# Kernel optimization log

Measured on AMD Instinct MI355X. Metric: run time of the kernel, lower is better.

The kernel has to match this reference:

```python
import jax, jax.numpy as jnp
import numpy as np

T, B, N, C, H, D = 4, 8, 1024, 512, 8, 64
EPS = 1e-5


def setup_inputs() -> dict:
    key = jax.random.key(0)
    ks = jax.random.split(key, 16)
    d = {"x": jax.random.normal(ks[0], (T, B, N, C), jnp.float32)}
    for i, nm in enumerate(["q", "k", "v", "p"]):
        kW, kmu, kvar = jax.random.split(ks[1 + i], 3)
        d[f"W{nm}"] = jax.random.normal(kW, (C, C), jnp.float32) * 0.02
        d[f"b{nm}"] = jnp.zeros((C,), jnp.float32)
        d[f"g{nm}"] = jnp.ones((C,), jnp.float32)
        d[f"beta{nm}"] = jnp.zeros((C,), jnp.float32)
        d[f"mu{nm}"] = jax.random.normal(kmu, (C,), jnp.float32) * 0.1
        d[f"var{nm}"] = jax.random.uniform(kvar, (C,), jnp.float32, 0.5, 1.5)
    return d


def _lin_bn(z, W, b, g, beta, mu, var):
    # nn.Linear over channel dim, then eval-mode BatchNorm1d per channel
    y = jnp.einsum('tbnc,dc->tbnd', z, W) + b
    return (y - mu) * (g * jax.lax.rsqrt(var + EPS)) + beta


def _to_heads(z):
    # (t,b,n,c) -> (t,b,h,n,d)
    return z.reshape(T, B, N, H, D).transpose(0, 1, 3, 2, 4)


def reference(x, Wq, bq, gq, betaq, muq, varq,
              Wk, bk, gk, betak, muk, vark,
              Wv, bv, gv, betav, muv, varv,
              Wp, bp, gp, betap, mup, varp):
    q = _to_heads(_lin_bn(x, Wq, bq, gq, betaq, muq, varq))
    k = _to_heads(_lin_bn(x, Wk, bk, gk, betak, muk, vark))
    v = _to_heads(_lin_bn(x, Wv, bv, gv, betav, muv, varv))
    # attention_linear variant: kv = (k^T @ v) / N ; y = q @ kv
    kv = jnp.einsum('tbhnd,tbhne->tbhde', k, v) / float(N)  # (t,b,h,d,d)
    y = jnp.einsum('tbhnd,tbhde->tbhne', q, kv)             # (t,b,h,n,d)
    y = y.transpose(0, 1, 3, 2, 4).reshape(T, B, N, C)
    return _lin_bn(y, Wp, bp, gp, betap, mup, varp)
```

## Files before the change

kernel.cpp:

```cpp
#include <hip/hip_runtime.h>

#define T_ 4
#define B_ 8
#define N_ 1024
#define C_ 512
#define H_ 8
#define D_ 64
#define M_ (T_*B_*N_)
#define TB_ (T_*B_)

typedef __bf16 bf16;
typedef __bf16 bf16x4 __attribute__((ext_vector_type(4)));
typedef __bf16 bf16x8 __attribute__((ext_vector_type(8)));
typedef float f32x4 __attribute__((ext_vector_type(4)));

__device__ __forceinline__ void gload16(const void* g, void* l) {
  __builtin_amdgcn_global_load_lds(
      (const __attribute__((address_space(1))) void*)g,
      (__attribute__((address_space(3))) void*)l, 16, 0, 0);
}

struct PtrPack { const float* p[24]; };

__global__ __launch_bounds__(256)
void cvt_prep(PtrPack pk, const float* __restrict__ x, bf16* __restrict__ xb,
              bf16* __restrict__ xT, float* __restrict__ spart,
              bf16* __restrict__ WB, float* __restrict__ BS,
              bf16* __restrict__ WqT) {
  const int t = threadIdx.x;
  __shared__ __align__(16) char smem[21120];
  if (blockIdx.x < 4096) {
    const int bid = blockIdx.x;
    const int tb = bid >> 7, nc = (bid >> 3) & 15, cc = bid & 7;
    float* lds = (float*)smem;
    float* sred = (float*)smem + 4160;
    const float* xbase = x + (size_t)tb * 524288 + (size_t)nc * 64 * 512 + cc * 64;
    bf16* xbb = xb + (size_t)tb * 524288 + (size_t)nc * 64 * 512 + cc * 64;
    bf16* xTb = xT + (size_t)tb * 524288 + (size_t)(cc * 64) * 1024 + nc * 64;
    const int rgrp = t >> 4, k = t & 15;
    float s0 = 0, s1 = 0, s2 = 0, s3 = 0;
#pragma unroll
    for (int p = 0; p < 4; p++) {
      int r = p * 16 + rgrp;
      float4 v = *(const float4*)(xbase + (size_t)r * 512 + k * 4);
      bf16x4 o; o[0]=(bf16)v.x; o[1]=(bf16)v.y; o[2]=(bf16)v.z; o[3]=(bf16)v.w;
      *(bf16x4*)(xbb + (size_t)r * 512 + k * 4) = o;
      lds[r*65 + k*4+0]=v.x; lds[r*65 + k*4+1]=v.y;
      lds[r*65 + k*4+2]=v.z; lds[r*65 + k*4+3]=v.w;
      s0 += v.x; s1 += v.y; s2 += v.z; s3 += v.w;
    }
    sred[rgrp*64 + k*4+0]=s0; sred[rgrp*64 + k*4+1]=s1;
    sred[rgrp*64 + k*4+2]=s2; sred[rgrp*64 + k*4+3]=s3;
    __syncthreads();
#pragma unroll
    for (int p = 0; p < 16; p++) {
      int c = p * 4 + (t >> 6), n = t & 63;
      xTb[(size_t)c * 1024 + n] = (bf16)lds[n*65 + c];
    }
    if (t < 64) {
      float tot = 0;
#pragma unroll
      for (int rg = 0; rg < 16; rg++) tot += sred[rg*64 + t];
      spart[(size_t)((tb*8 + cc)*16 + nc) * 64 + t] = tot;
    }
    return;
  }
  if (blockIdx.x < 6144) {
    const int e = blockIdx.x - 4096;
    const int mat = e >> 9, d = e & 511;
    const float* W    = pk.p[6*mat + 0];
    const float* b    = pk.p[6*mat + 1];
    const float* g    = pk.p[6*mat + 2];
    const float* beta = pk.p[6*mat + 3];
    const float* mu   = pk.p[6*mat + 4];
    const float* var  = pk.p[6*mat + 5];
    float s = g[d] * rsqrtf(var[d] + 1e-5f);
    if (t == 0) BS[mat*512 + d] = (b[d] - mu[d]) * s + beta[d];
    bf16* Wout = WB + (size_t)mat * 262144 + (size_t)d * 512;
    for (int c = t; c < 512; c += 256)
      Wout[c] = (bf16)(W[(size_t)d * 512 + c] * s);
    return;
  }
  const int e = blockIdx.x - 6144;
  const int di = e >> 3, ci = e & 7;
  float* lds = (float*)smem;
  const float* W = pk.p[0];
  const float* g = pk.p[2];
  const float* var = pk.p[5];
  const int rgrp = t >> 4, k = t & 15;
#pragma unroll
  for (int p = 0; p < 4; p++) {
    int r = p * 16 + rgrp;
    int d = di * 64 + r;
    float s = g[d] * rsqrtf(var[d] + 1e-5f);
    float4 v = *(const float4*)(W + (size_t)d * 512 + ci * 64 + k * 4);
    lds[r*65 + k*4+0] = v.x * s; lds[r*65 + k*4+1] = v.y * s;
    lds[r*65 + k*4+2] = v.z * s; lds[r*65 + k*4+3] = v.w * s;
  }
  __syncthreads();
#pragma unroll
  for (int p = 0; p < 16; p++) {
    int c = p * 4 + (t >> 6), dd = t & 63;
    WqT[(size_t)(ci*64 + c) * 512 + di*64 + dd] = (bf16)lds[dd*65 + c];
  }
}

__global__ __launch_bounds__(256)
void gram_ksvs(const bf16* __restrict__ xT, const bf16* __restrict__ WB,
               const float* __restrict__ spart, bf16* __restrict__ Gb,
               float* __restrict__ ksv) {
  const int t = threadIdx.x;
  __shared__ __align__(16) char smem[24576];
  if (blockIdx.x >= 640) {
    const int e = blockIdx.x - 640, tb = e >> 1, m = e & 1;
    float* sl = (float*)smem;
#pragma unroll
    for (int half = 0; half < 2; half++) {
      int c = t + half * 256, cc = c >> 6, cl = c & 63;
      float tot = 0;
#pragma unroll
      for (int ncf = 0; ncf < 16; ncf++)
        tot += spart[(size_t)((tb*8 + cc)*16 + ncf) * 64 + cl];
      sl[c] = tot;
    }
    __syncthreads();
#pragma unroll
    for (int half = 0; half < 2; half++) {
      int d = t + half * 256;
      const bf16* Wrow = WB + (size_t)(m + 1) * 262144 + (size_t)d * 512;
      float acc = 0;
      for (int k = 0; k < 512; k += 8) {
        bf16x8 wv = *(const bf16x8*)(Wrow + k);
#pragma unroll
        for (int i = 0; i < 8; i++) acc += (float)wv[i] * sl[k + i];
      }
      ksv[m * 16384 + tb * 512 + d] = acc;
    }
    return;
  }
  constexpr int K = 1024;
  const int bid = blockIdx.x;
  const int xcd = bid & 7, j9 = bid >> 3;
  const int bat = xcd + 8 * (j9 / 20);
  const int tile = j9 % 20;
  int mi, ni;
  if (tile < 8)       { mi = tile;          ni = 0; }
  else if (tile < 14) { mi = tile - 8 + 2;  ni = 1; }
  else if (tile < 18) { mi = tile - 14 + 4; ni = 2; }
  else                { mi = tile - 18 + 6; ni = 3; }
  const bf16* A = xT + (size_t)bat * 524288;
  const int m0 = mi * 64, n0 = ni * 128;
  bf16* As = (bf16*)smem;
  bf16* Bs = (bf16*)(smem + 8192);
  const int w = t >> 6, l = t & 63;
  const int wm = w >> 1, wn = w & 1;
  const int lr = l & 15, lq = l >> 4, l7 = l & 7, lh = l >> 3;
  const int srcc = (l7 ^ lh) * 8;
  f32x4 acc[2][4] = {};
  for (int kt = 0; kt < 16; kt++) {
#pragma unroll
    for (int i = 0; i < 2; i++) {
      int rb = w * 16 + i * 8;
      gload16(A + (size_t)(m0 + rb + lh) * K + kt * 64 + srcc, &As[rb * 64]);
    }
#pragma unroll
    for (int i = 0; i < 4; i++) {
      int rb = w * 32 + i * 8;
      gload16(A + (size_t)(n0 + rb + lh) * K + kt * 64 + srcc, &Bs[rb * 64]);
    }
    __syncthreads();
    bf16x8 af[2][2], bv[4][2];
#pragma unroll
    for (int f = 0; f < 2; f++) {
      int ra = wm * 32 + f * 16 + lr;
#pragma unroll
      for (int s = 0; s < 2; s++)
        af[f][s] = *(const bf16x8*)&As[ra * 64 + (((s*4+lq) ^ (ra & 7)) * 8)];
    }
#pragma unroll
    for (int f = 0; f < 4; f++) {
      int rb2 = wn * 64 + f * 16 + lr;
#pragma unroll
      for (int s = 0; s < 2; s++)
        bv[f][s] = *(const bf16x8*)&Bs[rb2 * 64 + (((s*4+lq) ^ (rb2 & 7)) * 8)];
    }
#pragma unroll
    for (int mt = 0; mt < 2; mt++)
#pragma unroll
      for (int nt = 0; nt < 4; nt++)
#pragma unroll
        for (int s = 0; s < 2; s++)
          acc[mt][nt] = __builtin_amdgcn_mfma_f32_16x16x32_bf16(
              af[mt][s], bv[nt][s], acc[mt][nt], 0, 0, 0);
    __syncthreads();
  }
  bf16* ob = Gb + (size_t)bat * 262144;
#pragma unroll
  for (int mt = 0; mt < 2; mt++)
#pragma unroll
    for (int nt = 0; nt < 4; nt++) {
      int j = n0 + wn * 64 + nt * 16 + lr;
      size_t mrow = (size_t)m0 + wm * 32 + mt * 16 + lq * 4;
#pragma unroll
      for (int r = 0; r < 4; r++)
        ob[(mrow + r) * 512 + j] = (bf16)acc[mt][nt][r];
    }
  bf16* TB = (bf16*)smem;
#pragma unroll
  for (int mt = 0; mt < 2; mt++)
#pragma unroll
    for (int nt = 0; nt < 4; nt++) {
      int a = wn * 64 + nt * 16 + lr;
#pragma unroll
      for (int r = 0; r < 4; r++) {
        int b = wm * 32 + mt * 16 + lq * 4 + r;
        TB[(a * 64 + b) ^ ((a & 7) << 3)] = (bf16)acc[mt][nt][r];
      }
    }
  __syncthreads();
  const int rowa = t >> 1, half = t & 1;
#pragma unroll
  for (int i = 0; i < 4; i++) {
    int c8 = half * 4 + i;
    bf16x8 v = *(const bf16x8*)&TB[(rowa * 64 + c8 * 8) ^ ((rowa & 7) << 3)];
    *(bf16x8*)(ob + (size_t)(n0 + rowa) * 512 + m0 + c8 * 8) = v;
  }
}

template <int NKT, int MTILES, bool BF16OUT, bool BIAS>
__global__ __launch_bounds__(256, 6)
void gemm_n(const bf16* __restrict__ Abase, size_t Astr,
            const bf16* __restrict__ Btbase, size_t Btstr,
            const float* __restrict__ BSb,
            bf16* __restrict__ ob, float* __restrict__ of, size_t Ostr) {
  constexpr int K = NKT * 64;
  constexpr int PERB = MTILES * 4;
  const int bid = blockIdx.x;
  const int xcd = bid & 7, j9 = bid >> 3;
  const int bat = xcd + 8 * (j9 / PERB);
  const int tile = j9 % PERB;
  const int mi = tile >> 2, ni = tile & 3;
  const bf16* A = Abase + (size_t)bat * Astr;
  const bf16* Bt = Btbase + (size_t)bat * Btstr;
  const int m0 = mi * 64, n0 = ni * 128;
  __shared__ __align__(16) bf16 As[64][64];
  __shared__ __align__(16) bf16 Bs[128][64];
  const int tid = threadIdx.x, w = tid >> 6, l = tid & 63;
  const int wm = w >> 1, wn = w & 1;
  const int lr = l & 15, lq = l >> 4, l7 = l & 7, lh = l >> 3;
  const int srcc = (l7 ^ lh) * 8;
  f32x4 acc[2][4] = {};
  for (int kt = 0; kt < NKT; kt++) {
#pragma unroll
    for (int i = 0; i < 2; i++) {
      int rb = w * 16 + i * 8;
      gload16(A + (size_t)(m0 + rb + lh) * K + kt * 64 + srcc, &As[rb][0]);
    }
#pragma unroll
    for (int i = 0; i < 4; i++) {
      int rb = w * 32 + i * 8;
      gload16(Bt + (size_t)(n0 + rb + lh) * K + kt * 64 + srcc, &Bs[rb][0]);
    }
    __syncthreads();
    bf16x8 af[2][2], bv[4][2];
#pragma unroll
    for (int f = 0; f < 2; f++) {
      int ra = wm * 32 + f * 16 + lr;
#pragma unroll
      for (int s = 0; s < 2; s++)
        af[f][s] = *(const bf16x8*)&As[ra][((s*4+lq) ^ (ra & 7)) * 8];
    }
#pragma unroll
    for (int f = 0; f < 4; f++) {
      int rb2 = wn * 64 + f * 16 + lr;
#pragma unroll
      for (int s = 0; s < 2; s++)
        bv[f][s] = *(const bf16x8*)&Bs[rb2][((s*4+lq) ^ (rb2 & 7)) * 8];
    }
#pragma unroll
    for (int mt = 0; mt < 2; mt++)
#pragma unroll
      for (int nt = 0; nt < 4; nt++)
#pragma unroll
        for (int s = 0; s < 2; s++)
          acc[mt][nt] = __builtin_amdgcn_mfma_f32_16x16x32_bf16(
              af[mt][s], bv[nt][s], acc[mt][nt], 0, 0, 0);
    __syncthreads();
  }

  float bja[4];
  if constexpr (BIAS) {
#pragma unroll
    for (int nt = 0; nt < 4; nt++) {
      int j = n0 + wn * 64 + nt * 16 + lr;
      bja[nt] = BSb[(size_t)bat * 512 + j];
    }
  }
#pragma unroll
  for (int mt = 0; mt < 2; mt++)
#pragma unroll
    for (int nt = 0; nt < 4; nt++) {
      int j = n0 + wn * 64 + nt * 16 + lr;
      size_t mrow = (size_t)m0 + wm * 32 + mt * 16 + lq * 4;
#pragma unroll
      for (int r = 0; r < 4; r++) {
        if constexpr (BF16OUT)
          ob[(size_t)bat * Ostr + (mrow + r) * 512 + j] = (bf16)acc[mt][nt][r];
        else
          of[(size_t)bat * Ostr + (mrow + r) * 512 + j] =
              acc[mt][nt][r] + (BIAS ? bja[nt] : 0.f);
      }
    }
}

__global__ __launch_bounds__(256, 6)
void gemm_vtc(const bf16* __restrict__ ZT, const bf16* __restrict__ WqT,
              const float* __restrict__ BS, const float* __restrict__ cpart,
              bf16* __restrict__ VT, float* __restrict__ cvec) {
  constexpr int K = 512;
  const int tid = threadIdx.x;
  if (blockIdx.x >= 1024) {
    const int tb = blockIdx.x - 1024;
#pragma unroll
    for (int half = 0; half < 2; half++) {
      int j = tid + half * 256;
      float s = BS[1536 + j];
#pragma unroll
      for (int h = 0; h < 8; h++) s += cpart[(size_t)(tb * 8 + h) * 512 + j];
      cvec[tb * 512 + j] = s;
    }
    return;
  }
  const int bid = blockIdx.x;
  const int xcd = bid & 7, j9 = bid >> 3;
  const int bat = xcd + 8 * (j9 >> 5);
  const int tile = j9 & 31;
  const int mi = tile >> 2, ni = tile & 3;
  const bf16* A = ZT + (size_t)bat * 262144;
  const int m0 = mi * 64, n0 = ni * 128;
  __shared__ __align__(16) bf16 As[64][64];
  __shared__ __align__(16) bf16 Bs[128][64];
  const int w = tid >> 6, l = tid & 63;
  const int wm = w >> 1, wn = w & 1;
  const int lr = l & 15, lq = l >> 4, l7 = l & 7, lh = l >> 3;
  const int srcc = (l7 ^ lh) * 8;
  f32x4 acc[2][4] = {};
  for (int kt = 0; kt < 8; kt++) {
#pragma unroll
    for (int i = 0; i < 2; i++) {
      int rb = w * 16 + i * 8;
      gload16(A + (size_t)(m0 + rb + lh) * K + kt * 64 + srcc, &As[rb][0]);
    }
#pragma unroll
    for (int i = 0; i < 4; i++) {
      int rb = w * 32 + i * 8;
      gload16(WqT + (size_t)(n0 + rb + lh) * K + kt * 64 + srcc, &Bs[rb][0]);
    }
    __syncthreads();
    bf16x8 af[2][2], bv[4][2];
#pragma unroll
    for (int f = 0; f < 2; f++) {
      int ra = wm * 32 + f * 16 + lr;
#pragma unroll
      for (int s = 0; s < 2; s++)
        af[f][s] = *(const bf16x8*)&As[ra][((s*4+lq) ^ (ra & 7)) * 8];
    }
#pragma unroll
    for (int f = 0; f < 4; f++) {
      int rb2 = wn * 64 + f * 16 + lr;
#pragma unroll
      for (int s = 0; s < 2; s++)
        bv[f][s] = *(const bf16x8*)&Bs[rb2][((s*4+lq) ^ (rb2 & 7)) * 8];
    }
#pragma unroll
    for (int mt = 0; mt < 2; mt++)
#pragma unroll
      for (int nt = 0; nt < 4; nt++)
#pragma unroll
        for (int s = 0; s < 2; s++)
          acc[mt][nt] = __builtin_amdgcn_mfma_f32_16x16x32_bf16(
              af[mt][s], bv[nt][s], acc[mt][nt], 0, 0, 0);
    __syncthreads();
  }
#pragma unroll
  for (int mt = 0; mt < 2; mt++)
#pragma unroll
    for (int nt = 0; nt < 4; nt++) {
      int j = n0 + wn * 64 + nt * 16 + lr;
      size_t mrow = (size_t)m0 + wm * 32 + mt * 16 + lq * 4;
#pragma unroll
      for (int r = 0; r < 4; r++)
        VT[(size_t)bat * 262144 + (mrow + r) * 512 + j] = (bf16)acc[mt][nt][r];
    }
}

__global__ __launch_bounds__(256)
void kvz(const bf16* __restrict__ KGb, const bf16* __restrict__ WB,
         const float* __restrict__ BS, const float* __restrict__ ksv,
         bf16* __restrict__ ZT, float* __restrict__ cpart) {
  const int gid = blockIdx.x, tb = gid >> 3, h = gid & 7;
  const int t = threadIdx.x, w = t >> 6, l = t & 63;
  const int lr = l & 15, lq = l >> 4;
  __shared__ __align__(16) bf16 kvb[4096];

  const bf16* KGrow = KGb + (size_t)tb * 262144 + (size_t)(64*h) * 512;
  const bf16* Vrow  = WB + 2u * 262144 + (size_t)(64*h) * 512;

  f32x4 acc2[4] = {};
  for (int ks = 0; ks < 16; ks++) {
    const int kc = ks * 32 + lq * 8;
    bf16x8 bv = *(const bf16x8*)(Vrow + (size_t)(w*16 + lr) * 512 + kc);
#pragma unroll
    for (int mf = 0; mf < 4; mf++) {
      bf16x8 af = *(const bf16x8*)(KGrow + (size_t)(mf*16 + lr) * 512 + kc);
      acc2[mf] = __builtin_amdgcn_mfma_f32_16x16x32_bf16(af, bv, acc2[mf], 0, 0, 0);
    }
  }
  {
    const float inv = 1.f / 1024.f;
    const int e = w * 16 + lr;
    const float vsh = ksv[16384 + tb * 512 + 64*h + e];
    const float bvh = BS[1024 + 64*h + e];
#pragma unroll
    for (int mf = 0; mf < 4; mf++)
#pragma unroll
      for (int r = 0; r < 4; r++) {
        int d = mf * 16 + lq * 4 + r;
        float ksh = ksv[tb * 512 + 64*h + d];
        float bkh = BS[512 + 64*h + d];
        float kv = (acc2[mf][r] + ksh * bvh + bkh * vsh) * inv + bkh * bvh;
        kvb[d * 64 + ((((e >> 3) ^ (d & 7)) * 8) + (e & 7))] = (bf16)kv;
      }
  }
  __syncthreads();

  f32x4 acc3[4][8] = {};
#pragma unroll
  for (int s = 0; s < 2; s++) {
    bf16x8 af3[4];
#pragma unroll
    for (int mf = 0; mf < 4; mf++) {
      int d = mf * 16 + lr;
      af3[mf] = *(const bf16x8*)&kvb[d * 64 + (((s*4+lq) ^ (d & 7)) * 8)];
    }
#pragma unroll
    for (int nf = 0; nf < 8; nf++) {
      int jj = w * 128 + nf * 16 + lr;
      bf16x8 b3 = *(const bf16x8*)(WB + 3u * 262144 + (size_t)jj * 512 +
                                   64*h + s * 32 + lq * 8);
#pragma unroll
      for (int mf = 0; mf < 4; mf++)
        acc3[mf][nf] = __builtin_amdgcn_mfma_f32_16x16x32_bf16(
            af3[mf], b3, acc3[mf][nf], 0, 0, 0);
    }
  }

  bf16* zbase = ZT + (size_t)tb * 262144 + 64*h;
#pragma unroll
  for (int nf = 0; nf < 8; nf++) {
    int jj = w * 128 + nf * 16 + lr;
    float cp = 0.f;
#pragma unroll
    for (int mf = 0; mf < 4; mf++) {
      bf16x4 o;
#pragma unroll
      for (int r = 0; r < 4; r++) {
        o[r] = (bf16)acc3[mf][nf][r];
        cp += acc3[mf][nf][r] * BS[64*h + mf*16 + lq*4 + r];
      }
      *(bf16x4*)(zbase + (size_t)jj * 512 + mf * 16 + lq * 4) = o;
    }
    cp += __shfl_xor(cp, 16);
    cp += __shfl_xor(cp, 32);
    if (lq == 0) cpart[(size_t)(tb * 8 + h) * 512 + jj] = cp;
  }
}

extern "C" void kernel_launch(void* const* d_in, const int* in_sizes, int n_in,
                              void* d_out, int out_size, void* d_ws, size_t ws_size,
                              hipStream_t stream) {
  const float* x = (const float*)d_in[0];
  char* ws = (char*)d_ws;
  bf16*  xb    = (bf16*)(ws + 0);
  bf16*  xT    = (bf16*)(ws + 33554432);
  bf16*  Gb    = (bf16*)(ws + 67108864);
  bf16*  KGb   = (bf16*)(ws + 83886080);
  bf16*  ZT    = (bf16*)(ws + 100663296);
  bf16*  VT    = (bf16*)(ws + 117440512);
  bf16*  WB    = (bf16*)(ws + 134217728);
  bf16*  WqT   = (bf16*)(ws + 136314880);
  float* BS    = (float*)(ws + 136839168);
  float* ksv   = (float*)(ws + 136847360);
  float* cpart = (float*)(ws + 136978432);
  float* cvec  = (float*)(ws + 137502720);
  float* spart = (float*)(ws + 137568256);
  (void)in_sizes; (void)n_in; (void)out_size; (void)ws_size;

  PtrPack pk;
  for (int i = 0; i < 24; i++) pk.p[i] = (const float*)d_in[1 + i];

  cvt_prep<<<6208, 256, 0, stream>>>(pk, x, xb, xT, spart, WB, BS, WqT);
  gram_ksvs<<<704, 256, 0, stream>>>(xT, WB, spart, Gb, ksv);
  gemm_n<8, 8, true, false><<<1024, 256, 0, stream>>>(
      WB + 262144, 0, Gb, 262144, nullptr, KGb, nullptr, 262144);
  kvz<<<256, 256, 0, stream>>>(KGb, WB, BS, ksv, ZT, cpart);
  gemm_vtc<<<1056, 256, 0, stream>>>(ZT, WqT, BS, cpart, VT, cvec);
  gemm_n<8, 16, false, true><<<2048, 256, 0, stream>>>(
      xb, 524288, VT, 262144, cvec, nullptr, (float*)d_out, 524288);
}
```

Measured before the change: 135.7 us.

## Fuse fp32-to-bf16 conversion of x into final output GEMM

```diff
diff --git a/kernel.cpp b/kernel.cpp
--- a/kernel.cpp
+++ b/kernel.cpp
@@ -23,7 +23,7 @@
 struct PtrPack { const float* p[24]; };
 
 __global__ __launch_bounds__(256)
-void cvt_prep(PtrPack pk, const float* __restrict__ x, bf16* __restrict__ xb,
+void cvt_prep(PtrPack pk, const float* __restrict__ x,
               bf16* __restrict__ xT, float* __restrict__ spart,
               bf16* __restrict__ WB, float* __restrict__ BS,
               bf16* __restrict__ WqT) {
@@ -35,7 +35,6 @@
     float* lds = (float*)smem;
     float* sred = (float*)smem + 4160;
     const float* xbase = x + (size_t)tb * 524288 + (size_t)nc * 64 * 512 + cc * 64;
-    bf16* xbb = xb + (size_t)tb * 524288 + (size_t)nc * 64 * 512 + cc * 64;
     bf16* xTb = xT + (size_t)tb * 524288 + (size_t)(cc * 64) * 1024 + nc * 64;
     const int rgrp = t >> 4, k = t & 15;
     float s0 = 0, s1 = 0, s2 = 0, s3 = 0;
@@ -43,8 +42,6 @@
     for (int p = 0; p < 4; p++) {
       int r = p * 16 + rgrp;
       float4 v = *(const float4*)(xbase + (size_t)r * 512 + k * 4);
-      bf16x4 o; o[0]=(bf16)v.x; o[1]=(bf16)v.y; o[2]=(bf16)v.z; o[3]=(bf16)v.w;
-      *(bf16x4*)(xbb + (size_t)r * 512 + k * 4) = o;
       lds[r*65 + k*4+0]=v.x; lds[r*65 + k*4+1]=v.y;
       lds[r*65 + k*4+2]=v.z; lds[r*65 + k*4+3]=v.w;
       s0 += v.x; s1 += v.y; s2 += v.z; s3 += v.w;
@@ -313,6 +310,89 @@
     }
 }
 
+__global__ __launch_bounds__(256, 5)
+void gemm_ox(const float* __restrict__ x, const bf16* __restrict__ VTb,
+             const float* __restrict__ cvec, float* __restrict__ of) {
+  constexpr int K = 512, NKT = 8, PERB = 64;
+  const int bid = blockIdx.x;
+  const int xcd = bid & 7, j9 = bid >> 3;
+  const int bat = xcd + 8 * (j9 / PERB);
+  const int tile = j9 % PERB;
+  const int mi = tile >> 2, ni = tile & 3;
+  const float* A = x + (size_t)bat * 524288;
+  const bf16* Bt = VTb + (size_t)bat * 262144;
+  const int m0 = mi * 64, n0 = ni * 128;
+  __shared__ __align__(16) bf16 As[64][64];
+  __shared__ __align__(16) bf16 Bs[128][64];
+  const int tid = threadIdx.x, w = tid >> 6, l = tid & 63;
+  const int wm = w >> 1, wn = w & 1;
+  const int lr = l & 15, lq = l >> 4, l7 = l & 7, lh = l >> 3;
+  const int srcc = (l7 ^ lh) * 8;
+  const int ach = tid & 7;
+  const int arow = tid >> 3;
+  f32x4 acc[2][4] = {};
+  for (int kt = 0; kt < NKT; kt++) {
+#pragma unroll
+    for (int i = 0; i < 2; i++) {
+      int r = i * 32 + arow;
+      const float* src = A + (size_t)(m0 + r) * 512 + kt * 64 + ach * 8;
+      float4 v0 = *(const float4*)(src);
+      float4 v1 = *(const float4*)(src + 4);
+      bf16x8 o;
+      o[0]=(bf16)v0.x; o[1]=(bf16)v0.y; o[2]=(bf16)v0.z; o[3]=(bf16)v0.w;
+      o[4]=(bf16)v1.x; o[5]=(bf16)v1.y; o[6]=(bf16)v1.z; o[7]=(bf16)v1.w;
+      *(bf16x8*)&As[r][((ach ^ (r & 7)) * 8)] = o;
+    }
+#pragma unroll
+    for (int i = 0; i < 4; i++) {
+      int rb = w * 32 + i * 8;
+      gload16(Bt + (size_t)(n0 + rb + lh) * K + kt * 64 + srcc, &Bs[rb][0]);
+    }
+    __syncthreads();
+    bf16x8 af[2][2], bv[4][2];
+#pragma unroll
+    for (int f = 0; f < 2; f++) {
+      int ra = wm * 32 + f * 16 + lr;
+#pragma unroll
+      for (int s = 0; s < 2; s++)
+        af[f][s] = *(const bf16x8*)&As[ra][((s*4+lq) ^ (ra & 7)) * 8];
+    }
+#pragma unroll
+    for (int f = 0; f < 4; f++) {
+      int rb2 = wn * 64 + f * 16 + lr;
+#pragma unroll
+      for (int s = 0; s < 2; s++)
+        bv[f][s] = *(const bf16x8*)&Bs[rb2][((s*4+lq) ^ (rb2 & 7)) * 8];
+    }
+#pragma unroll
+    for (int mt = 0; mt < 2; mt++)
+#pragma unroll
+      for (int nt = 0; nt < 4; nt++)
+#pragma unroll
+        for (int s = 0; s < 2; s++)
+          acc[mt][nt] = __builtin_amdgcn_mfma_f32_16x16x32_bf16(
+              af[mt][s], bv[nt][s], acc[mt][nt], 0, 0, 0);
+    __syncthreads();
+  }
+
+  float bja[4];
+#pragma unroll
+  for (int nt = 0; nt < 4; nt++) {
+    int j = n0 + wn * 64 + nt * 16 + lr;
+    bja[nt] = cvec[(size_t)bat * 512 + j];
+  }
+#pragma unroll
+  for (int mt = 0; mt < 2; mt++)
+#pragma unroll
+    for (int nt = 0; nt < 4; nt++) {
+      int j = n0 + wn * 64 + nt * 16 + lr;
+      size_t mrow = (size_t)m0 + wm * 32 + mt * 16 + lq * 4;
+#pragma unroll
+      for (int r = 0; r < 4; r++)
+        of[(size_t)bat * 524288 + (mrow + r) * 512 + j] = acc[mt][nt][r] + bja[nt];
+    }
+}
+
 __global__ __launch_bounds__(256, 6)
 void gemm_vtc(const bf16* __restrict__ ZT, const bf16* __restrict__ WqT,
               const float* __restrict__ BS, const float* __restrict__ cpart,
@@ -481,7 +561,6 @@
                               hipStream_t stream) {
   const float* x = (const float*)d_in[0];
   char* ws = (char*)d_ws;
-  bf16*  xb    = (bf16*)(ws + 0);
   bf16*  xT    = (bf16*)(ws + 33554432);
   bf16*  Gb    = (bf16*)(ws + 67108864);
   bf16*  KGb   = (bf16*)(ws + 83886080);
@@ -499,12 +578,11 @@
   PtrPack pk;
   for (int i = 0; i < 24; i++) pk.p[i] = (const float*)d_in[1 + i];
 
-  cvt_prep<<<6208, 256, 0, stream>>>(pk, x, xb, xT, spart, WB, BS, WqT);
+  cvt_prep<<<6208, 256, 0, stream>>>(pk, x, xT, spart, WB, BS, WqT);
   gram_ksvs<<<704, 256, 0, stream>>>(xT, WB, spart, Gb, ksv);
   gemm_n<8, 8, true, false><<<1024, 256, 0, stream>>>(
       WB + 262144, 0, Gb, 262144, nullptr, KGb, nullptr, 262144);
   kvz<<<256, 256, 0, stream>>>(KGb, WB, BS, ksv, ZT, cpart);
   gemm_vtc<<<1056, 256, 0, stream>>>(ZT, WqT, BS, cpart, VT, cvec);
-  gemm_n<8, 16, false, true><<<2048, 256, 0, stream>>>(
-      xb, 524288, VT, 262144, cvec, nullptr, (float*)d_out, 524288);
-}
+  gemm_ox<<<2048, 256, 0, stream>>>(x, VT, cvec, (float*)d_out);
+}
```

Measured after the change: 133.9 us. Within noise of the previous version (-1.4%).
